# Kernel optimization log

Hardware: AMD Instinct MI355X
Metric: run time of the kernel (lower is better)

## Reference

```python
import jax, jax.numpy as jnp
import numpy as np

TOP_K = 2

def setup_inputs() -> dict:
    key = jax.random.key(0)
    ks = jax.random.split(key, 5)
    B, S, D, E, R, H = 4, 2048, 1024, 8, 128, 4096
    s = 0.02
    return {
        "hidden_states": jax.random.normal(ks[0], (B, S, D), jnp.float32),
        "w_route": jax.random.normal(ks[1], (E, D, R), jnp.float32) * s,
        "w3": jax.random.normal(ks[2], (E, D, H), jnp.float32) * s,
        "wr2h": jax.random.normal(ks[3], (E, R, H), jnp.float32) * s,
        "wh2d": jax.random.normal(ks[4], (E, H, D), jnp.float32) * s,
    }

def reference(hidden_states, w_route, w3, wr2h, wh2d):
    B, S, D = hidden_states.shape
    E = w_route.shape[0]
    x = hidden_states.reshape(-1, D)                      # [N, D]
    N = x.shape[0]
    # per-expert routing activations (also reused as w1_state inside experts)
    acts = jnp.einsum('nd,edr->ner', x, w_route)          # [N, E, R]
    norms = jnp.linalg.norm(acts, axis=-1)                # [N, E] router logits
    probs = jax.nn.softmax(norms.astype(jnp.float32), axis=-1)
    topw, sel = jax.lax.top_k(probs, TOP_K)               # [N, k]
    topw = topw / topw.sum(axis=-1, keepdims=True)
    topw = topw.astype(x.dtype)
    # dense combine weights: routing weight if expert selected, else 0
    combine = jnp.zeros((N, E), x.dtype).at[jnp.arange(N)[:, None], sel].add(topw)
    out = jnp.zeros_like(x)
    for e in range(E):  # fixed small expert count
        h = (x @ w3[e]) * jax.nn.silu(acts[:, e, :] @ wr2h[e])  # [N, H]
        out = out + (h @ wh2d[e]) * combine[:, e:e + 1]
    final = out.reshape(B, S, D)
    # load balancing loss on the router logits (expert_act_norms)
    mask = jax.nn.one_hot(sel, E, dtype=jnp.float32)      # [N, k, E]
    tokens_per_expert = mask.mean(axis=0)                 # [k, E]
    router_prob_per_expert = probs.mean(axis=0)           # [E]
    bl_loss = jnp.sum(tokens_per_expert * router_prob_per_expert[None, :]) * E
    return final, norms, bl_loss
```

## Files before the change

### kernel.cpp

```cpp
#include <hip/hip_runtime.h>


#define DEV static __device__ __forceinline__

typedef float  f32x4  __attribute__((ext_vector_type(4)));
typedef __bf16 bf16x8 __attribute__((ext_vector_type(8)));

DEV unsigned short f2bf(float f) {
  union { float f; unsigned u; } v; v.f = f;
  unsigned r = v.u + 0x7fffu + ((v.u >> 16) & 1u);
  return (unsigned short)(r >> 16);
}
DEV float bf2f(unsigned short b) {
  union { unsigned u; float f; } v; v.u = ((unsigned)b) << 16;
  return v.f;
}

DEV void gll16(const void* g, void* l) {
  __builtin_amdgcn_global_load_lds(
      (const __attribute__((address_space(1))) unsigned int*)g,
      (__attribute__((address_space(3))) unsigned int*)l, 16, 0, 0);
}

DEV f32x4 mfma16(bf16x8 a, bf16x8 b, f32x4 c) {
  return __builtin_amdgcn_mfma_f32_16x16x32_bf16(a, b, c, 0, 0, 0);
}

DEV void stage_linear(const unsigned short* base, size_t pitch, int k0,
                      unsigned short* lds, int tid) {
  int wq = tid >> 6, lane = tid & 63;
#pragma unroll
  for (int i = 0; i < 4; ++i) {
    int s = wq * 256 + i * 64 + lane;
    int row = s >> 3, b = s & 7;
    int bb = b ^ (row & 7);
    const unsigned short* g = base + (size_t)row * pitch + (size_t)(k0 + bb * 8);
    gll16(g, lds + (size_t)(wq * 256 + i * 64) * 8);
  }
}

DEV void stage_gather(const unsigned short* base, size_t pitch, size_t colOff,
                      int k0, const int* toks, unsigned short* lds, int tid) {
  int wq = tid >> 6, lane = tid & 63;
#pragma unroll
  for (int i = 0; i < 4; ++i) {
    int s = wq * 256 + i * 64 + lane;
    int row = s >> 3, b = s & 7;
    int bb = b ^ (row & 7);
    const unsigned short* g =
        base + (size_t)toks[row] * pitch + colOff + (size_t)(k0 + bb * 8);
    gll16(g, lds + (size_t)(wq * 256 + i * 64) * 8);
  }
}

DEV bf16x8 frag_read(const unsigned short* lds, int row, int kb) {
  int off = row * 128 + ((kb * 2) ^ ((row & 7) << 4));
  return *(const bf16x8*)((const char*)lds + off);
}

DEV void mfma_block(const unsigned short* A, const unsigned short* B,
                    f32x4 (&acc)[4][4], int wm, int wn, int lg, int lc) {
#pragma unroll
  for (int ks = 0; ks < 2; ++ks) {
    int kb = ks * 32 + lg * 8;
    bf16x8 af[4], bff[4];
#pragma unroll
    for (int i = 0; i < 4; ++i) {
      af[i]  = frag_read(A, wm * 64 + i * 16 + lc, kb);
      bff[i] = frag_read(B, wn * 64 + i * 16 + lc, kb);
    }
#pragma unroll
    for (int mf = 0; mf < 4; ++mf)
#pragma unroll
      for (int nf = 0; nf < 4; ++nf)
        acc[mf][nf] = mfma16(af[mf], bff[nf], acc[mf][nf]);
  }
}


__global__ __launch_bounds__(256) void k_cast_x(const float* __restrict__ x,
    unsigned short* __restrict__ xh, unsigned short* __restrict__ xl) {
  int stride = gridDim.x * blockDim.x;
  for (int i = blockIdx.x * blockDim.x + threadIdx.x; i < 8192 * 1024 / 4;
       i += stride) {
    float4 v = ((const float4*)x)[i];
    ushort4 h, l;
    h.x = f2bf(v.x); l.x = f2bf(v.x - bf2f(h.x));
    h.y = f2bf(v.y); l.y = f2bf(v.y - bf2f(h.y));
    h.z = f2bf(v.z); l.z = f2bf(v.z - bf2f(h.z));
    h.w = f2bf(v.w); l.w = f2bf(v.w - bf2f(h.w));
    ((ushort4*)xh)[i] = h;
    ((ushort4*)xl)[i] = l;
  }
}

__global__ void k_zero(int* cnt, float* probsum) {
  int t = threadIdx.x;
  if (t < 16) cnt[t] = 0;
  if (t < 8)  probsum[t] = 0.f;
}

__global__ __launch_bounds__(256) void k_transp(const float* __restrict__ src,
    unsigned short* __restrict__ dst, int K, int N) {
  int ntn = N >> 6;
  int kt = blockIdx.x / ntn, nt = blockIdx.x % ntn;
  int e = blockIdx.y;
  __shared__ float tl[64][65];
  const float* s = src + (size_t)e * K * N;
  unsigned short* d = dst + (size_t)e * N * K;
  int tid = threadIdx.x;
  int c4 = (tid & 15) * 4, rr = tid >> 4;
#pragma unroll
  for (int p = 0; p < 4; ++p) {
    int row = rr + p * 16;
    float4 v = *(const float4*)(s + (size_t)(kt * 64 + row) * N + nt * 64 + c4);
    tl[row][c4] = v.x; tl[row][c4 + 1] = v.y;
    tl[row][c4 + 2] = v.z; tl[row][c4 + 3] = v.w;
  }
  __syncthreads();
#pragma unroll
  for (int p = 0; p < 4; ++p) {
    int n = rr + p * 16;
    ushort4 o;
    o.x = f2bf(tl[c4 + 0][n]); o.y = f2bf(tl[c4 + 1][n]);
    o.z = f2bf(tl[c4 + 2][n]); o.w = f2bf(tl[c4 + 3][n]);
    *(ushort4*)(d + (size_t)(nt * 64 + n) * K + kt * 64 + c4) = o;
  }
}

__global__ __launch_bounds__(256) void k_transp_split(const float* __restrict__ src,
    unsigned short* __restrict__ dh, unsigned short* __restrict__ dl, int K, int N) {
  int ntn = N >> 6;
  int kt = blockIdx.x / ntn, nt = blockIdx.x % ntn;
  int e = blockIdx.y;
  __shared__ float tl[64][65];
  const float* s = src + (size_t)e * K * N;
  size_t dbase = (size_t)e * N * K;
  int tid = threadIdx.x;
  int c4 = (tid & 15) * 4, rr = tid >> 4;
#pragma unroll
  for (int p = 0; p < 4; ++p) {
    int row = rr + p * 16;
    float4 v = *(const float4*)(s + (size_t)(kt * 64 + row) * N + nt * 64 + c4);
    tl[row][c4] = v.x; tl[row][c4 + 1] = v.y;
    tl[row][c4 + 2] = v.z; tl[row][c4 + 3] = v.w;
  }
  __syncthreads();
#pragma unroll
  for (int p = 0; p < 4; ++p) {
    int n = rr + p * 16;
    ushort4 oh, ol;
#pragma unroll
    for (int i = 0; i < 4; ++i) {
      float v = tl[c4 + i][n];
      unsigned short hh = f2bf(v);
      unsigned short ll = f2bf(v - bf2f(hh));
      ((unsigned short*)&oh)[i] = hh;
      ((unsigned short*)&ol)[i] = ll;
    }
    *(ushort4*)(dh + dbase + (size_t)(nt * 64 + n) * K + kt * 64 + c4) = oh;
    *(ushort4*)(dl + dbase + (size_t)(nt * 64 + n) * K + kt * 64 + c4) = ol;
  }
}

__global__ __launch_bounds__(256) void k_route_gemm(
    const unsigned short* __restrict__ xh, const unsigned short* __restrict__ xl,
    const unsigned short* __restrict__ wrh_t, const unsigned short* __restrict__ wrl_t,
    unsigned short* __restrict__ acts, float* __restrict__ norms_out) {
  __shared__ __align__(16) unsigned short Ah[128 * 64], Al[128 * 64];
  __shared__ __align__(16) unsigned short Bh[128 * 64], Bl[128 * 64];
  __shared__ float ssq_s[128][2];
  int tid = threadIdx.x;
  int mt = blockIdx.x, e = blockIdx.y;
  int wq = tid >> 6, lane = tid & 63;
  int wm = wq >> 1, wn = wq & 1, lg = lane >> 4, lc = lane & 15;
  f32x4 acc[4][4] = {};
  const unsigned short* ah_src = xh + (size_t)mt * 128 * 1024;
  const unsigned short* al_src = xl + (size_t)mt * 128 * 1024;
  const unsigned short* bh_src = wrh_t + (size_t)e * 128 * 1024;
  const unsigned short* bl_src = wrl_t + (size_t)e * 128 * 1024;
  for (int kt = 0; kt < 16; ++kt) {
    int k0 = kt * 64;
    stage_linear(ah_src, 1024, k0, Ah, tid);
    stage_linear(al_src, 1024, k0, Al, tid);
    stage_linear(bh_src, 1024, k0, Bh, tid);
    stage_linear(bl_src, 1024, k0, Bl, tid);
    __syncthreads();
#pragma unroll
    for (int ks = 0; ks < 2; ++ks) {
      int kb = ks * 32 + lg * 8;
      bf16x8 ahf[4], alf[4], bhf[4], blf[4];
#pragma unroll
      for (int i = 0; i < 4; ++i) {
        ahf[i] = frag_read(Ah, wm * 64 + i * 16 + lc, kb);
        alf[i] = frag_read(Al, wm * 64 + i * 16 + lc, kb);
        bhf[i] = frag_read(Bh, wn * 64 + i * 16 + lc, kb);
        blf[i] = frag_read(Bl, wn * 64 + i * 16 + lc, kb);
      }
#pragma unroll
      for (int mf = 0; mf < 4; ++mf)
#pragma unroll
        for (int nf = 0; nf < 4; ++nf) {
          acc[mf][nf] = mfma16(ahf[mf], bhf[nf], acc[mf][nf]);
          acc[mf][nf] = mfma16(alf[mf], bhf[nf], acc[mf][nf]);
          acc[mf][nf] = mfma16(ahf[mf], blf[nf], acc[mf][nf]);
        }
    }
    __syncthreads();
  }
  float ssq[4][4];
#pragma unroll
  for (int mf = 0; mf < 4; ++mf)
#pragma unroll
    for (int r = 0; r < 4; ++r) ssq[mf][r] = 0.f;
#pragma unroll
  for (int mf = 0; mf < 4; ++mf)
#pragma unroll
    for (int nf = 0; nf < 4; ++nf)
#pragma unroll
      for (int r = 0; r < 4; ++r) {
        float v = acc[mf][nf][r];
        int row = wm * 64 + mf * 16 + lg * 4 + r;
        int col = wn * 64 + nf * 16 + lc;
        acts[(size_t)(mt * 128 + row) * 1024 + e * 128 + col] = f2bf(v);
        ssq[mf][r] += v * v;
      }
#pragma unroll
  for (int mf = 0; mf < 4; ++mf)
#pragma unroll
    for (int r = 0; r < 4; ++r) {
      float s = ssq[mf][r];
      s += __shfl_xor(s, 1); s += __shfl_xor(s, 2);
      s += __shfl_xor(s, 4); s += __shfl_xor(s, 8);
      if (lc == 0) ssq_s[wm * 64 + mf * 16 + lg * 4 + r][wn] = s;
    }
  __syncthreads();
  if (tid < 128) {
    float s = ssq_s[tid][0] + ssq_s[tid][1];
    norms_out[(size_t)(mt * 128 + tid) * 8 + e] = sqrtf(s);
  }
}

__global__ __launch_bounds__(256) void k_router(const float* __restrict__ norms,
    float* __restrict__ topw, int* __restrict__ sel,
    int* __restrict__ cnt, float* __restrict__ probsum) {
  __shared__ float ps_s[8];
  __shared__ int cnt_s[16];
  int tid = threadIdx.x;
  if (tid < 8)  ps_s[tid] = 0.f;
  if (tid < 16) cnt_s[tid] = 0;
  __syncthreads();
  int n = blockIdx.x * 256 + tid;
  float p[8], mx = -3.4e38f;
#pragma unroll
  for (int e = 0; e < 8; ++e) { p[e] = norms[(size_t)n * 8 + e]; mx = fmaxf(mx, p[e]); }
  float s = 0.f;
#pragma unroll
  for (int e = 0; e < 8; ++e) { p[e] = __expf(p[e] - mx); s += p[e]; }
  float inv = 1.f / s;
  int i1 = 0; float v1 = p[0];
#pragma unroll
  for (int e = 1; e < 8; ++e) if (p[e] > v1) { v1 = p[e]; i1 = e; }
  int i2 = -1; float v2 = -1.f;
#pragma unroll
  for (int e = 0; e < 8; ++e) if (e != i1 && p[e] > v2) { v2 = p[e]; i2 = e; }
  float wsum = v1 + v2;
  topw[n * 2 + 0] = v1 / wsum;
  topw[n * 2 + 1] = v2 / wsum;
  sel[n * 2 + 0] = i1;
  sel[n * 2 + 1] = i2;
  atomicAdd(&cnt_s[i1], 1);
  atomicAdd(&cnt_s[8 + i2], 1);
#pragma unroll
  for (int e = 0; e < 8; ++e) atomicAdd(&ps_s[e], p[e] * inv);
  __syncthreads();
  if (tid < 8)  atomicAdd(&probsum[tid], ps_s[tid]);
  if (tid < 16) atomicAdd(&cnt[tid], cnt_s[tid]);
}

__global__ void k_plan(const int* __restrict__ cnt, const float* __restrict__ probsum,
                       int* __restrict__ offs, int* __restrict__ fill,
                       int4* __restrict__ tilemap, float* __restrict__ bl_out) {
  for (int k = 0; k < 2; ++k) {
    int pos = 0, t = 0;
    for (int e = 0; e < 8; ++e) {
      int c = cnt[k * 8 + e];
      offs[k * 8 + e] = pos;
      int ntl = (c + 127) >> 7;
      for (int i = 0; i < ntl; ++i) {
        int rr = c - i * 128; if (rr > 128) rr = 128;
        tilemap[k * 72 + t] = make_int4(e, pos + i * 128, rr, 0);
        ++t;
      }
      pos += c;
    }
    for (; t < 72; ++t) tilemap[k * 72 + t] = make_int4(0, pos, 0, 0);
  }
  for (int i = 0; i < 16; ++i) fill[i] = 0;
  float bl = 0.f;
  for (int e = 0; e < 8; ++e)
    bl += ((float)(cnt[e] + cnt[8 + e]) / 8192.f) * (probsum[e] / 8192.f);
  *bl_out = bl * 8.f;
}

__global__ __launch_bounds__(256) void k_fill(const int* __restrict__ sel,
    const int* __restrict__ offs, int* __restrict__ fill, int* __restrict__ list01) {
  int n = blockIdx.x * 256 + threadIdx.x;
#pragma unroll
  for (int k = 0; k < 2; ++k) {
    int e = sel[n * 2 + k];
    int pos = atomicAdd(&fill[k * 8 + e], 1);
    list01[k * 8192 + offs[k * 8 + e] + pos] = n;
  }
}

__global__ __launch_bounds__(256) void k_gemm1(
    const unsigned short* __restrict__ xh, const unsigned short* __restrict__ acts,
    const unsigned short* __restrict__ w3t, const unsigned short* __restrict__ wr2h_t,
    const int* __restrict__ list, const int4* __restrict__ tilemap, int tile_lo,
    unsigned short* __restrict__ hbuf) {
  __shared__ __align__(16) unsigned short A[128 * 64], B[128 * 64];
  __shared__ int toks[128];
  int4 ent = tilemap[tile_lo + blockIdx.x];
  int e = ent.x, posbase = ent.y, rows = ent.z;
  if (rows == 0) return;
  int hbase = tilemap[tile_lo].y;
  int bn = blockIdx.y;
  int tid = threadIdx.x;
  if (tid < 128) {
    int rr = tid < rows ? tid : rows - 1;
    toks[tid] = list[posbase + rr];
  }
  __syncthreads();
  int wq = tid >> 6, lane = tid & 63;
  int wm = wq >> 1, wn = wq & 1, lg = lane >> 4, lc = lane & 15;
  f32x4 acc_a[4][4] = {};
  const unsigned short* bsrc = w3t + ((size_t)e * 4096 + bn * 128) * 1024;
  for (int kt = 0; kt < 16; ++kt) {
    int k0 = kt * 64;
    stage_gather(xh, 1024, 0, k0, toks, A, tid);
    stage_linear(bsrc, 1024, k0, B, tid);
    __syncthreads();
    mfma_block(A, B, acc_a, wm, wn, lg, lc);
    __syncthreads();
  }
  f32x4 acc_s[4][4] = {};
  const unsigned short* b2src = wr2h_t + ((size_t)e * 4096 + bn * 128) * 128;
  for (int kt = 0; kt < 2; ++kt) {
    int k0 = kt * 64;
    stage_gather(acts, 1024, (size_t)e * 128, k0, toks, A, tid);
    stage_linear(b2src, 128, k0, B, tid);
    __syncthreads();
    mfma_block(A, B, acc_s, wm, wn, lg, lc);
    __syncthreads();
  }
  size_t hrow0 = (size_t)(posbase - hbase);
#pragma unroll
  for (int mf = 0; mf < 4; ++mf)
#pragma unroll
    for (int nf = 0; nf < 4; ++nf)
#pragma unroll
      for (int r = 0; r < 4; ++r) {
        int row = wm * 64 + mf * 16 + lg * 4 + r;
        if (row < rows) {
          int col = wn * 64 + nf * 16 + lc;
          float sv = acc_s[mf][nf][r];
          float hv = acc_a[mf][nf][r] * (sv / (1.f + __expf(-sv)));
          hbuf[(hrow0 + row) * 4096 + (size_t)bn * 128 + col] = f2bf(hv);
        }
      }
}

__global__ __launch_bounds__(256) void k_gemm2(
    const unsigned short* __restrict__ hbuf, const unsigned short* __restrict__ wh2dt,
    const int* __restrict__ list, const float* __restrict__ topw,
    const int4* __restrict__ tilemap, int tile_lo, int slot,
    float* __restrict__ out) {
  __shared__ __align__(16) unsigned short A[128 * 64], B[128 * 64];
  __shared__ int toks[128];
  __shared__ float wr_s[128];
  int4 ent = tilemap[tile_lo + blockIdx.x];
  int e = ent.x, posbase = ent.y, rows = ent.z;
  if (rows == 0) return;
  int hbase = tilemap[tile_lo].y;
  int bn = blockIdx.y;
  int tid = threadIdx.x;
  if (tid < 128) {
    int rr = tid < rows ? tid : rows - 1;
    int t = list[posbase + rr];
    toks[tid] = t;
    wr_s[tid] = topw[t * 2 + slot];
  }
  __syncthreads();
  int wq = tid >> 6, lane = tid & 63;
  int wm = wq >> 1, wn = wq & 1, lg = lane >> 4, lc = lane & 15;
  f32x4 acc[4][4] = {};
  const unsigned short* asrc = hbuf + (size_t)(posbase - hbase) * 4096;
  const unsigned short* bsrc = wh2dt + ((size_t)e * 1024 + bn * 128) * 4096;
  for (int kt = 0; kt < 64; ++kt) {
    int k0 = kt * 64;
    stage_linear(asrc, 4096, k0, A, tid);
    stage_linear(bsrc, 4096, k0, B, tid);
    __syncthreads();
    mfma_block(A, B, acc, wm, wn, lg, lc);
    __syncthreads();
  }
#pragma unroll
  for (int mf = 0; mf < 4; ++mf)
#pragma unroll
    for (int nf = 0; nf < 4; ++nf)
#pragma unroll
      for (int r = 0; r < 4; ++r) {
        int row = wm * 64 + mf * 16 + lg * 4 + r;
        if (row < rows) {
          int col = wn * 64 + nf * 16 + lc;
          float v = acc[mf][nf][r] * wr_s[row];
          size_t o = (size_t)toks[row] * 1024 + bn * 128 + col;
          if (slot == 0) out[o] = v; else out[o] += v;
        }
      }
}


extern "C" void kernel_launch(void* const* d_in, const int* in_sizes, int n_in,
                              void* d_out, int out_size, void* d_ws, size_t ws_size,
                              hipStream_t stream) {
  (void)in_sizes; (void)n_in; (void)out_size;
  const float* x      = (const float*)d_in[0];
  const float* wroute = (const float*)d_in[1];
  const float* w3     = (const float*)d_in[2];
  const float* wr2h   = (const float*)d_in[3];
  const float* wh2d   = (const float*)d_in[4];
  float* out = (float*)d_out;

  char* ws = (char*)d_ws;
  size_t off = 0;
  auto carve = [&](size_t bytes) -> void* {
    void* p = ws + off; off += (bytes + 255) & ~(size_t)255; return p;
  };
  unsigned short* xh     = (unsigned short*)carve((size_t)8192 * 1024 * 2);
  unsigned short* xl     = (unsigned short*)carve((size_t)8192 * 1024 * 2);
  unsigned short* wrh_t  = (unsigned short*)carve((size_t)8 * 128 * 1024 * 2);
  unsigned short* wrl_t  = (unsigned short*)carve((size_t)8 * 128 * 1024 * 2);
  unsigned short* w3t    = (unsigned short*)carve((size_t)8 * 4096 * 1024 * 2);
  unsigned short* wr2h_t = (unsigned short*)carve((size_t)8 * 4096 * 128 * 2);
  unsigned short* wh2dt  = (unsigned short*)carve((size_t)8 * 1024 * 4096 * 2);
  unsigned short* acts   = (unsigned short*)carve((size_t)8192 * 1024 * 2);
  int*   list01 = (int*)carve(2 * 8192 * 4);
  int*   sel    = (int*)carve(8192 * 2 * 4);
  float* topw   = (float*)carve(8192 * 2 * 4);
  int*   ctr    = (int*)carve(4096);
  int* cnt = ctr; int* fill = ctr + 16; int* offs = ctr + 32;
  float* probsum = (float*)(ctr + 48);
  int4* tilemap = (int4*)(ctr + 64);

  int nchunk = 0, tpc = 0;
  for (int c = 1; c <= 8; c <<= 1) {
    int t = (72 + c - 1) / c;
    if (off + (size_t)t * 128 * 4096 * 2 <= ws_size) { nchunk = c; tpc = t; break; }
  }
  if (!nchunk) return;
  unsigned short* hbuf = (unsigned short*)(ws + off);

  float* norms_out = out + 8388608;
  float* bl_out    = out + 8454144;

  k_cast_x<<<2048, 256, 0, stream>>>(x, xh, xl);
  k_zero<<<1, 64, 0, stream>>>(cnt, probsum);
  k_transp<<<dim3(16 * 64, 8), 256, 0, stream>>>(w3, w3t, 1024, 4096);
  k_transp<<<dim3(64 * 16, 8), 256, 0, stream>>>(wh2d, wh2dt, 4096, 1024);
  k_transp<<<dim3(2 * 64, 8), 256, 0, stream>>>(wr2h, wr2h_t, 128, 4096);
  k_transp_split<<<dim3(16 * 2, 8), 256, 0, stream>>>(wroute, wrh_t, wrl_t, 1024, 128);
  k_route_gemm<<<dim3(64, 8), 256, 0, stream>>>(xh, xl, wrh_t, wrl_t, acts, norms_out);
  k_router<<<32, 256, 0, stream>>>(norms_out, topw, sel, cnt, probsum);
  k_plan<<<1, 1, 0, stream>>>(cnt, probsum, offs, fill, tilemap, bl_out);
  k_fill<<<32, 256, 0, stream>>>(sel, offs, fill, list01);

  for (int slot = 0; slot < 2; ++slot) {
    for (int c = 0; c < nchunk; ++c) {
      int tile_lo = c * tpc;
      int nt = (72 - tile_lo < tpc) ? (72 - tile_lo) : tpc;
      if (nt <= 0) break;
      k_gemm1<<<dim3(nt, 32), 256, 0, stream>>>(
          xh, acts, w3t, wr2h_t, list01 + slot * 8192, tilemap + slot * 72,
          tile_lo, hbuf);
      k_gemm2<<<dim3(nt, 8), 256, 0, stream>>>(
          hbuf, wh2dt, list01 + slot * 8192, topw, tilemap + slot * 72,
          tile_lo, slot, out);
    }
  }
}
```

Baseline: 900.3 us.

## Double-buffer expert GEMMs, merge both routing slots, swizzle blocks across XCDs

Both expert GEMM kernels now use two LDS buffers, so the next K-slice is loaded while MFMAs run on the current one, and one barrier per step is removed. The two top-k slots are merged into a single 144-tile schedule and launched together, with the output zeroed up front and accumulated through atomicAdd. Routing weights are gathered into a per-slot list during the fill step. Workgroup ids are remapped with an XCD-aware swizzle so tiles that share weights land on the same die. This costs more LDS per block, which may reduce occupancy, plus atomic traffic on the output and a memset pass.

```diff
diff --git a/kernel.cpp b/kernel.cpp
--- a/kernel.cpp
+++ b/kernel.cpp
@@ -24,6 +24,11 @@
 
 DEV f32x4 mfma16(bf16x8 a, bf16x8 b, f32x4 c) {
   return __builtin_amdgcn_mfma_f32_16x16x32_bf16(a, b, c, 0, 0, 0);
+}
+
+DEV int xcd_swz(int bid, int nwg) {
+  int q = nwg >> 3;
+  return (bid & 7) * q + (bid >> 3);
 }
 
 DEV void stage_linear(const unsigned short* base, size_t pitch, int k0,
@@ -281,21 +286,22 @@
 __global__ void k_plan(const int* __restrict__ cnt, const float* __restrict__ probsum,
                        int* __restrict__ offs, int* __restrict__ fill,
                        int4* __restrict__ tilemap, float* __restrict__ bl_out) {
+  int t = 0;
   for (int k = 0; k < 2; ++k) {
-    int pos = 0, t = 0;
+    int pos = 0;
     for (int e = 0; e < 8; ++e) {
       int c = cnt[k * 8 + e];
       offs[k * 8 + e] = pos;
       int ntl = (c + 127) >> 7;
       for (int i = 0; i < ntl; ++i) {
         int rr = c - i * 128; if (rr > 128) rr = 128;
-        tilemap[k * 72 + t] = make_int4(e, pos + i * 128, rr, 0);
+        tilemap[t] = make_int4(e, k * 8192 + pos + i * 128, rr, 0);
         ++t;
       }
       pos += c;
     }
-    for (; t < 72; ++t) tilemap[k * 72 + t] = make_int4(0, pos, 0, 0);
-  }
+  }
+  for (; t < 144; ++t) tilemap[t] = make_int4(0, 0, 0, 0);
   for (int i = 0; i < 16; ++i) fill[i] = 0;
   float bl = 0.f;
   for (int e = 0; e < 8; ++e)
@@ -304,13 +310,16 @@
 }
 
 __global__ __launch_bounds__(256) void k_fill(const int* __restrict__ sel,
-    const int* __restrict__ offs, int* __restrict__ fill, int* __restrict__ list01) {
+    const float* __restrict__ topw, const int* __restrict__ offs,
+    int* __restrict__ fill, int* __restrict__ list01, float* __restrict__ wlist) {
   int n = blockIdx.x * 256 + threadIdx.x;
 #pragma unroll
   for (int k = 0; k < 2; ++k) {
     int e = sel[n * 2 + k];
     int pos = atomicAdd(&fill[k * 8 + e], 1);
-    list01[k * 8192 + offs[k * 8 + e] + pos] = n;
+    int idx = k * 8192 + offs[k * 8 + e] + pos;
+    list01[idx] = n;
+    wlist[idx] = topw[n * 2 + k];
   }
 }
 
@@ -318,14 +327,15 @@
     const unsigned short* __restrict__ xh, const unsigned short* __restrict__ acts,
     const unsigned short* __restrict__ w3t, const unsigned short* __restrict__ wr2h_t,
     const int* __restrict__ list, const int4* __restrict__ tilemap, int tile_lo,
-    unsigned short* __restrict__ hbuf) {
-  __shared__ __align__(16) unsigned short A[128 * 64], B[128 * 64];
+    int nt, unsigned short* __restrict__ hbuf) {
+  __shared__ __align__(16) unsigned short SA[2 * 128 * 64];
+  __shared__ __align__(16) unsigned short SB[2 * 128 * 64];
   __shared__ int toks[128];
-  int4 ent = tilemap[tile_lo + blockIdx.x];
+  int wg = xcd_swz(blockIdx.x, nt * 32);
+  int tileIdx = wg >> 5, bn = wg & 31;
+  int4 ent = tilemap[tile_lo + tileIdx];
   int e = ent.x, posbase = ent.y, rows = ent.z;
   if (rows == 0) return;
-  int hbase = tilemap[tile_lo].y;
-  int bn = blockIdx.y;
   int tid = threadIdx.x;
   if (tid < 128) {
     int rr = tid < rows ? tid : rows - 1;
@@ -336,25 +346,30 @@
   int wm = wq >> 1, wn = wq & 1, lg = lane >> 4, lc = lane & 15;
   f32x4 acc_a[4][4] = {};
   const unsigned short* bsrc = w3t + ((size_t)e * 4096 + bn * 128) * 1024;
-  for (int kt = 0; kt < 16; ++kt) {
-    int k0 = kt * 64;
-    stage_gather(xh, 1024, 0, k0, toks, A, tid);
-    stage_linear(bsrc, 1024, k0, B, tid);
+  stage_gather(xh, 1024, 0, 0, toks, SA, tid);
+  stage_linear(bsrc, 1024, 0, SB, tid);
+  __syncthreads();
+  int cur = 0;
+  for (int kt = 0; kt < 15; ++kt) {
+    int nxt = cur ^ 1;
+    stage_gather(xh, 1024, 0, (kt + 1) * 64, toks, SA + nxt * 8192, tid);
+    stage_linear(bsrc, 1024, (kt + 1) * 64, SB + nxt * 8192, tid);
+    mfma_block(SA + cur * 8192, SB + cur * 8192, acc_a, wm, wn, lg, lc);
     __syncthreads();
-    mfma_block(A, B, acc_a, wm, wn, lg, lc);
-    __syncthreads();
-  }
+    cur = nxt;
+  }
+  mfma_block(SA + cur * 8192, SB + cur * 8192, acc_a, wm, wn, lg, lc);
+  __syncthreads();
   f32x4 acc_s[4][4] = {};
   const unsigned short* b2src = wr2h_t + ((size_t)e * 4096 + bn * 128) * 128;
-  for (int kt = 0; kt < 2; ++kt) {
-    int k0 = kt * 64;
-    stage_gather(acts, 1024, (size_t)e * 128, k0, toks, A, tid);
-    stage_linear(b2src, 128, k0, B, tid);
-    __syncthreads();
-    mfma_block(A, B, acc_s, wm, wn, lg, lc);
-    __syncthreads();
-  }
-  size_t hrow0 = (size_t)(posbase - hbase);
+  stage_gather(acts, 1024, (size_t)e * 128, 0, toks, SA, tid);
+  stage_linear(b2src, 128, 0, SB, tid);
+  stage_gather(acts, 1024, (size_t)e * 128, 64, toks, SA + 8192, tid);
+  stage_linear(b2src, 128, 64, SB + 8192, tid);
+  __syncthreads();
+  mfma_block(SA, SB, acc_s, wm, wn, lg, lc);
+  mfma_block(SA + 8192, SB + 8192, acc_s, wm, wn, lg, lc);
+  size_t hrow0 = (size_t)tileIdx * 128;
 #pragma unroll
   for (int mf = 0; mf < 4; ++mf)
 #pragma unroll
@@ -373,38 +388,43 @@
 
 __global__ __launch_bounds__(256) void k_gemm2(
     const unsigned short* __restrict__ hbuf, const unsigned short* __restrict__ wh2dt,
-    const int* __restrict__ list, const float* __restrict__ topw,
-    const int4* __restrict__ tilemap, int tile_lo, int slot,
+    const int* __restrict__ list, const float* __restrict__ wlist,
+    const int4* __restrict__ tilemap, int tile_lo, int nt,
     float* __restrict__ out) {
-  __shared__ __align__(16) unsigned short A[128 * 64], B[128 * 64];
+  __shared__ __align__(16) unsigned short SA[2 * 128 * 64];
+  __shared__ __align__(16) unsigned short SB[2 * 128 * 64];
   __shared__ int toks[128];
   __shared__ float wr_s[128];
-  int4 ent = tilemap[tile_lo + blockIdx.x];
+  int wg = xcd_swz(blockIdx.x, nt * 8);
+  int tileIdx = wg >> 3, bn = wg & 7;
+  int4 ent = tilemap[tile_lo + tileIdx];
   int e = ent.x, posbase = ent.y, rows = ent.z;
   if (rows == 0) return;
-  int hbase = tilemap[tile_lo].y;
-  int bn = blockIdx.y;
   int tid = threadIdx.x;
   if (tid < 128) {
     int rr = tid < rows ? tid : rows - 1;
-    int t = list[posbase + rr];
-    toks[tid] = t;
-    wr_s[tid] = topw[t * 2 + slot];
+    toks[tid] = list[posbase + rr];
+    wr_s[tid] = wlist[posbase + rr];
   }
   __syncthreads();
   int wq = tid >> 6, lane = tid & 63;
   int wm = wq >> 1, wn = wq & 1, lg = lane >> 4, lc = lane & 15;
   f32x4 acc[4][4] = {};
-  const unsigned short* asrc = hbuf + (size_t)(posbase - hbase) * 4096;
+  const unsigned short* asrc = hbuf + (size_t)tileIdx * 128 * 4096;
   const unsigned short* bsrc = wh2dt + ((size_t)e * 1024 + bn * 128) * 4096;
-  for (int kt = 0; kt < 64; ++kt) {
-    int k0 = kt * 64;
-    stage_linear(asrc, 4096, k0, A, tid);
-    stage_linear(bsrc, 4096, k0, B, tid);
+  stage_linear(asrc, 4096, 0, SA, tid);
+  stage_linear(bsrc, 4096, 0, SB, tid);
+  __syncthreads();
+  int cur = 0;
+  for (int kt = 0; kt < 63; ++kt) {
+    int nxt = cur ^ 1;
+    stage_linear(asrc, 4096, (kt + 1) * 64, SA + nxt * 8192, tid);
+    stage_linear(bsrc, 4096, (kt + 1) * 64, SB + nxt * 8192, tid);
+    mfma_block(SA + cur * 8192, SB + cur * 8192, acc, wm, wn, lg, lc);
     __syncthreads();
-    mfma_block(A, B, acc, wm, wn, lg, lc);
-    __syncthreads();
-  }
+    cur = nxt;
+  }
+  mfma_block(SA + cur * 8192, SB + cur * 8192, acc, wm, wn, lg, lc);
 #pragma unroll
   for (int mf = 0; mf < 4; ++mf)
 #pragma unroll
@@ -415,8 +435,7 @@
         if (row < rows) {
           int col = wn * 64 + nf * 16 + lc;
           float v = acc[mf][nf][r] * wr_s[row];
-          size_t o = (size_t)toks[row] * 1024 + bn * 128 + col;
-          if (slot == 0) out[o] = v; else out[o] += v;
+          atomicAdd(out + (size_t)toks[row] * 1024 + bn * 128 + col, v);
         }
       }
 }
@@ -447,24 +466,27 @@
   unsigned short* wh2dt  = (unsigned short*)carve((size_t)8 * 1024 * 4096 * 2);
   unsigned short* acts   = (unsigned short*)carve((size_t)8192 * 1024 * 2);
   int*   list01 = (int*)carve(2 * 8192 * 4);
+  float* wlist  = (float*)carve(2 * 8192 * 4);
   int*   sel    = (int*)carve(8192 * 2 * 4);
   float* topw   = (float*)carve(8192 * 2 * 4);
-  int*   ctr    = (int*)carve(4096);
+  int*   ctr    = (int*)carve(8192);
   int* cnt = ctr; int* fill = ctr + 16; int* offs = ctr + 32;
   float* probsum = (float*)(ctr + 48);
   int4* tilemap = (int4*)(ctr + 64);
 
-  int nchunk = 0, tpc = 0;
-  for (int c = 1; c <= 8; c <<= 1) {
-    int t = (72 + c - 1) / c;
-    if (off + (size_t)t * 128 * 4096 * 2 <= ws_size) { nchunk = c; tpc = t; break; }
-  }
-  if (!nchunk) return;
+  size_t avail = ws_size > off ? ws_size - off : 0;
+  int tpc = 0;
+  const int cands[8] = {144, 72, 48, 36, 24, 18, 12, 9};
+  for (int i = 0; i < 8; ++i) {
+    if ((size_t)cands[i] * 128 * 4096 * 2 <= avail) { tpc = cands[i]; break; }
+  }
+  if (!tpc) return;
   unsigned short* hbuf = (unsigned short*)(ws + off);
 
   float* norms_out = out + 8388608;
   float* bl_out    = out + 8454144;
 
+  hipMemsetAsync(out, 0, (size_t)8388608 * 4, stream);
   k_cast_x<<<2048, 256, 0, stream>>>(x, xh, xl);
   k_zero<<<1, 64, 0, stream>>>(cnt, probsum);
   k_transp<<<dim3(16 * 64, 8), 256, 0, stream>>>(w3, w3t, 1024, 4096);
@@ -474,19 +496,15 @@
   k_route_gemm<<<dim3(64, 8), 256, 0, stream>>>(xh, xl, wrh_t, wrl_t, acts, norms_out);
   k_router<<<32, 256, 0, stream>>>(norms_out, topw, sel, cnt, probsum);
   k_plan<<<1, 1, 0, stream>>>(cnt, probsum, offs, fill, tilemap, bl_out);
-  k_fill<<<32, 256, 0, stream>>>(sel, offs, fill, list01);
-
-  for (int slot = 0; slot < 2; ++slot) {
-    for (int c = 0; c < nchunk; ++c) {
-      int tile_lo = c * tpc;
-      int nt = (72 - tile_lo < tpc) ? (72 - tile_lo) : tpc;
-      if (nt <= 0) break;
-      k_gemm1<<<dim3(nt, 32), 256, 0, stream>>>(
-          xh, acts, w3t, wr2h_t, list01 + slot * 8192, tilemap + slot * 72,
-          tile_lo, hbuf);
-      k_gemm2<<<dim3(nt, 8), 256, 0, stream>>>(
-          hbuf, wh2dt, list01 + slot * 8192, topw, tilemap + slot * 72,
-          tile_lo, slot, out);
-    }
-  }
-}
+  k_fill<<<32, 256, 0, stream>>>(sel, topw, offs, fill, list01, wlist);
+
+  int nchunk = (144 + tpc - 1) / tpc;
+  for (int c = 0; c < nchunk; ++c) {
+    int tile_lo = c * tpc;
+    int nt = 144 - tile_lo < tpc ? 144 - tile_lo : tpc;
+    k_gemm1<<<nt * 32, 256, 0, stream>>>(
+        xh, acts, w3t, wr2h_t, list01, tilemap, tile_lo, nt, hbuf);
+    k_gemm2<<<nt * 8, 256, 0, stream>>>(
+        hbuf, wh2dt, list01, wlist, tilemap, tile_lo, nt, out);
+  }
+}
```

Measured after the change: 889.9 us. About the same (-1.2%).
